# Kernel tuning notes

Hardware: AMD Instinct MI355X
Metric: run time of the kernel (lower is better)

## Reference

```python
import jax, jax.numpy as jnp
import numpy as np

IMG = 800.0
STRIDES = (4, 8, 16, 32)
SIZES = (32.0, 64.0, 128.0, 256.0)
RATIOS = (0.5, 1.0, 2.0)
A = 3
PRE_NMS_K = 1000
POST_NMS = 512
NMS_TH = 0.7
POOL = 7
_MEAN = np.array([0.485, 0.456, 0.406], np.float32).reshape(3, 1, 1)
_STD = np.array([0.229, 0.224, 0.225], np.float32).reshape(3, 1, 1)


def _conv(x, w, stride=1):
    # x: [C,H,W], w: [O,I,kh,kw]
    return jax.lax.conv_general_dilated(x[None], w, (stride, stride), 'SAME',
                                        dimension_numbers=('NCHW', 'OIHW', 'NCHW'))[0]


def _make_anchors(fh, fw, stride, size):
    cy = (np.arange(fh, dtype=np.float32) + 0.5) * stride
    cx = (np.arange(fw, dtype=np.float32) + 0.5) * stride
    ws = np.array([size / np.sqrt(r) for r in RATIOS], np.float32)
    hs = np.array([size * np.sqrt(r) for r in RATIOS], np.float32)
    gy, gx = np.meshgrid(cy, cx, indexing='ij')
    x1 = gx[..., None] - ws / 2; y1 = gy[..., None] - hs / 2
    x2 = gx[..., None] + ws / 2; y2 = gy[..., None] + hs / 2
    return jnp.asarray(np.stack([x1, y1, x2, y2], -1).reshape(-1, 4))  # [fh*fw*A,4]


def _decode(anchors, deltas):
    aw = anchors[:, 2] - anchors[:, 0]; ah = anchors[:, 3] - anchors[:, 1]
    acx = anchors[:, 0] + aw * 0.5; acy = anchors[:, 1] + ah * 0.5
    dw = jnp.clip(deltas[:, 2], -4.0, 4.0); dh = jnp.clip(deltas[:, 3], -4.0, 4.0)
    cx = acx + deltas[:, 0] * aw; cy = acy + deltas[:, 1] * ah
    w = aw * jnp.exp(dw); h = ah * jnp.exp(dh)
    boxes = jnp.stack([cx - w * 0.5, cy - h * 0.5, cx + w * 0.5, cy + h * 0.5], -1)
    return jnp.clip(boxes, 0.0, IMG)


def _nms(boxes, scores, iou_th, max_out):
    # Greedy NMS with fixed output size (jit-compatible).
    x1, y1, x2, y2 = boxes[:, 0], boxes[:, 1], boxes[:, 2], boxes[:, 3]
    areas = (x2 - x1) * (y2 - y1)

    def body(i, state):
        s, keep = state
        idx = jnp.argmax(s)
        keep = keep.at[i].set(idx)
        ix1 = jnp.maximum(x1, x1[idx]); iy1 = jnp.maximum(y1, y1[idx])
        ix2 = jnp.minimum(x2, x2[idx]); iy2 = jnp.minimum(y2, y2[idx])
        inter = jnp.maximum(ix2 - ix1, 0.0) * jnp.maximum(iy2 - iy1, 0.0)
        iou = inter / (areas + areas[idx] - inter + 1e-6)
        return jnp.where(iou > iou_th, -jnp.inf, s), keep

    _, keep = jax.lax.fori_loop(0, max_out, body, (scores, jnp.zeros(max_out, jnp.int32)))
    return keep


def _roi_align(feat, rois, scale):
    # feat: [C,H,W]; rois: [N,4] in image coords; bilinear, 1 sample per bin.
    C, H, W = feat.shape
    n = rois.shape[0]
    x1 = rois[:, 0] * scale; y1 = rois[:, 1] * scale
    bw = (rois[:, 2] - rois[:, 0]) * scale / POOL
    bh = (rois[:, 3] - rois[:, 1]) * scale / POOL
    j = jnp.arange(POOL, dtype=feat.dtype) + 0.5
    gx = jnp.broadcast_to((x1[:, None] + j * bw[:, None] - 0.5)[:, None, :], (n, POOL, POOL))
    gy = jnp.broadcast_to((y1[:, None] + j * bh[:, None] - 0.5)[:, :, None], (n, POOL, POOL))
    fx = jnp.clip(jnp.floor(gx), 0.0, W - 1); fy = jnp.clip(jnp.floor(gy), 0.0, H - 1)
    x0 = fx.astype(jnp.int32); y0 = fy.astype(jnp.int32)
    x1i = jnp.minimum(x0 + 1, W - 1); y1i = jnp.minimum(y0 + 1, H - 1)
    wx = jnp.clip(gx - fx, 0.0, 1.0); wy = jnp.clip(gy - fy, 0.0, 1.0)
    v = (feat[:, y0, x0] * (1 - wy) * (1 - wx) + feat[:, y0, x1i] * (1 - wy) * wx
         + feat[:, y1i, x0] * wy * (1 - wx) + feat[:, y1i, x1i] * wy * wx)  # [C,N,P,P]
    return jnp.transpose(v, (1, 0, 2, 3))  # [N,C,P,P]


def _forward(x, stem_w, c2_w, c3_w, c4_w, c5_w, fpn2_w, fpn3_w, fpn4_w, fpn5_w,
             rpn_w, rpn_cls_w, rpn_box_w, fc1_w, fc1_b, fc2_w, fc2_b,
             cls_w, cls_b, breg_w, breg_b):
    x = (x - _MEAN) / _STD  # ImageNet normalize
    h = jax.nn.relu(_conv(x, stem_w, 2))      # [64,400,400]
    c2 = jax.nn.relu(_conv(h, c2_w, 2))       # [256,200,200] stride 4
    c3 = jax.nn.relu(_conv(c2, c3_w, 2))      # stride 8
    c4 = jax.nn.relu(_conv(c3, c4_w, 2))      # stride 16
    c5 = jax.nn.relu(_conv(c4, c5_w, 2))      # stride 32
    feats = [_conv(c2, fpn2_w), _conv(c3, fpn3_w), _conv(c4, fpn4_w), _conv(c5, fpn5_w)]

    boxes_l, scores_l = [], []
    for lvl, f in enumerate(feats):
        t = jax.nn.relu(_conv(f, rpn_w))
        fh, fw = f.shape[1], f.shape[2]
        logits = jnp.transpose(_conv(t, rpn_cls_w), (1, 2, 0)).reshape(-1)  # [fh*fw*A]
        deltas = jnp.transpose(_conv(t, rpn_box_w).reshape(A, 4, fh, fw), (2, 3, 0, 1)).reshape(-1, 4)
        anchors = _make_anchors(fh, fw, STRIDES[lvl], SIZES[lvl])
        dec = _decode(anchors, deltas)
        k = min(PRE_NMS_K, logits.shape[0])
        sc, idx = jax.lax.top_k(logits, k)
        boxes_l.append(dec[idx]); scores_l.append(sc)

    boxes = jnp.concatenate(boxes_l, 0)
    scores = jnp.concatenate(scores_l, 0)
    keep = _nms(boxes, scores, NMS_TH, POST_NMS)
    props = boxes[keep]  # [POST_NMS,4]

    pooled = _roi_align(feats[0], props, 1.0 / STRIDES[0])  # [N,256,7,7]
    v = pooled.reshape(POST_NMS, -1)
    v = jax.nn.relu(v @ fc1_w + fc1_b)
    v = jax.nn.relu(v @ fc2_w + fc2_b)
    return v @ cls_w + cls_b, v @ breg_w + breg_b, props, scores[keep]


def setup_inputs() -> dict:
    key = jax.random.key(0)
    ks = jax.random.split(key, 18)

    def he(k, shape):
        fan_in = int(np.prod(shape[1:])) if len(shape) == 4 else shape[0]
        return jax.random.normal(k, shape, jnp.float32) * float(np.sqrt(2.0 / fan_in))

    inp = {'x': jax.random.uniform(ks[0], (3, 800, 800), jnp.float32)}
    inp['stem_w'] = he(ks[1], (64, 3, 7, 7))
    inp['c2_w'] = he(ks[2], (256, 64, 3, 3))
    for i, name in enumerate(['c3_w', 'c4_w', 'c5_w', 'fpn2_w', 'fpn3_w', 'fpn4_w', 'fpn5_w', 'rpn_w']):
        inp[name] = he(ks[3 + i], (256, 256, 3, 3))
    inp['rpn_cls_w'] = he(ks[11], (3, 256, 1, 1))
    inp['rpn_box_w'] = he(ks[12], (12, 256, 1, 1))
    inp['fc1_w'] = he(ks[13], (12544, 1024)); inp['fc1_b'] = jnp.zeros((1024,), jnp.float32)
    inp['fc2_w'] = he(ks[14], (1024, 1024)); inp['fc2_b'] = jnp.zeros((1024,), jnp.float32)
    inp['cls_w'] = he(ks[15], (1024, 2)); inp['cls_b'] = jnp.zeros((2,), jnp.float32)
    inp['breg_w'] = he(ks[16], (1024, 8)); inp['breg_b'] = jnp.zeros((8,), jnp.float32)
    return inp


def reference(x, stem_w, c2_w, c3_w, c4_w, c5_w, fpn2_w, fpn3_w, fpn4_w, fpn5_w,
              rpn_w, rpn_cls_w, rpn_box_w, fc1_w, fc1_b, fc2_w, fc2_b,
              cls_w, cls_b, breg_w, breg_b):
    return _forward(x, stem_w, c2_w, c3_w, c4_w, c5_w, fpn2_w, fpn3_w, fpn4_w, fpn5_w,
                    rpn_w, rpn_cls_w, rpn_box_w, fc1_w, fc1_b, fc2_w, fc2_b,
                    cls_w, cls_b, breg_w, breg_b)
```

## Files before the change

kernel.cpp:

```cpp
#include <hip/hip_runtime.h>
#include <math.h>


#define DI __device__ __forceinline__

typedef short short8 __attribute__((ext_vector_type(8)));
typedef float float16v __attribute__((ext_vector_type(16)));

DI unsigned fkey(float f) {
  unsigned u = __float_as_uint(f);
  return (u & 0x80000000u) ? ~u : (u | 0x80000000u);
}

DI unsigned short f2bf(float f) {
  unsigned u = __float_as_uint(f);
  unsigned r = (u + 0x7FFFu + ((u >> 16) & 1u)) >> 16;
  return (unsigned short)r;
}

__global__ __launch_bounds__(256) void stem_conv(const float* __restrict__ x,
                                                 const float* __restrict__ w,
                                                 float* __restrict__ out) {
  __shared__ float tin[3 * 37 * 37];
  __shared__ float tw[4 * 147];
  const int x0 = blockIdx.x * 16, y0 = blockIdx.y * 16, co0 = blockIdx.z * 4;
  const int tid = threadIdx.x;
  for (int i = tid; i < 4 * 147; i += 256) tw[i] = w[co0 * 147 + i];
  const int ix0 = x0 * 2 - 2, iy0 = y0 * 2 - 2;
  const float mean[3] = {0.485f, 0.456f, 0.406f};
  const float stdv[3] = {0.229f, 0.224f, 0.225f};
  for (int i = tid; i < 3 * 37 * 37; i += 256) {
    int c = i / 1369, r = i % 1369, yy = r / 37, xx = r % 37;
    int gy = iy0 + yy, gx = ix0 + xx;
    float v = 0.f;
    if ((unsigned)gy < 800u && (unsigned)gx < 800u)
      v = __fdiv_rn(__fsub_rn(x[c * 640000 + gy * 800 + gx], mean[c]), stdv[c]);
    tin[i] = v;
  }
  __syncthreads();
  const int tx = tid & 15, ty = tid >> 4;
  float acc[4] = {0.f, 0.f, 0.f, 0.f};
  for (int c = 0; c < 3; ++c)
    for (int ky = 0; ky < 7; ++ky)
#pragma unroll
      for (int kx = 0; kx < 7; ++kx) {
        float v = tin[c * 1369 + (ty * 2 + ky) * 37 + (tx * 2 + kx)];
#pragma unroll
        for (int co = 0; co < 4; ++co)
          acc[co] = fmaf(v, tw[co * 147 + c * 49 + ky * 7 + kx], acc[co]);
      }
  int ox = x0 + tx, oy = y0 + ty;
#pragma unroll
  for (int co = 0; co < 4; ++co)
    out[(size_t)(co0 + co) * 160000 + oy * 400 + ox] = fmaxf(acc[co], 0.f);
}

__global__ void repack_w32(const float* __restrict__ w,
                           float* __restrict__ wpk, int Cin) {
  int i = blockIdx.x * 256 + threadIdx.x;
  int total = 16 * Cin * 9 * 16;
  if (i >= total) return;
  int co = i & 15;
  int r = i >> 4;
  int kk = r % 9;
  int r2 = r / 9;
  int ci = r2 % Cin;
  int z = r2 / Cin;
  wpk[i] = w[((size_t)(z * 16 + co) * Cin + ci) * 9 + kk];
}

template <bool RELU>
__global__ __launch_bounds__(256) void conv32_db(
    const float* __restrict__ in, const float* __restrict__ wpk,
    float* __restrict__ out, int Cin, int Hin, int Win, int Hout, int Wout) {
  __shared__ __align__(16) float tin2[2][5120];
  const int tid = threadIdx.x;
  const int tx = tid & 15, ty = tid >> 4;
  const int x0 = blockIdx.x * 32, y0 = blockIdx.y * 16;
  const int ix0 = x0 - 1, iy0 = y0 - 1;
  const size_t HWin = (size_t)Hin * Win;

  int goff[20];
#pragma unroll
  for (int j = 0; j < 20; ++j) {
    int e = j * 256 + tid;
    int c = e / 612, r = e % 612;
    int yy = r / 34, xx = r % 34;
    int gy = iy0 + yy, gx = ix0 + xx;
    bool ok = (e < 4896) && ((unsigned)gy < (unsigned)Hin) &&
              ((unsigned)gx < (unsigned)Win);
    goff[j] = ok ? (int)((size_t)c * HWin + (size_t)gy * Win + gx) : -1;
  }

  float acc0[16], acc1[16];
#pragma unroll
  for (int co = 0; co < 16; ++co) { acc0[co] = 0.f; acc1[co] = 0.f; }

  float stg[20];
#pragma unroll
  for (int j = 0; j < 20; ++j)
    stg[j] = (goff[j] >= 0) ? in[goff[j]] : 0.f;
#pragma unroll
  for (int j = 0; j < 20; ++j) tin2[0][j * 256 + tid] = stg[j];
  __syncthreads();

  int buf = 0;
  for (int cb = 0; cb < Cin; cb += 8) {
    const bool more = (cb + 8) < Cin;
    if (more) {
      const float* gsrc = in + (size_t)(cb + 8) * HWin;
#pragma unroll
      for (int j = 0; j < 20; ++j)
        stg[j] = (goff[j] >= 0) ? gsrc[goff[j]] : 0.f;
    }
    for (int ci = 0; ci < 8; ++ci) {
      const float4* wq = (const float4*)(wpk +
          ((size_t)blockIdx.z * Cin + (size_t)(cb + ci)) * 144);
#pragma unroll
      for (int ky = 0; ky < 3; ++ky) {
        const float* tb = &tin2[buf][ci * 612 + (ty + ky) * 34 + 2 * tx];
        float2 d0 = *(const float2*)tb;
        float2 d1 = *(const float2*)(tb + 2);
#pragma unroll
        for (int kx = 0; kx < 3; ++kx) {
          float v0 = (kx == 0) ? d0.x : (kx == 1) ? d0.y : d1.x;
          float v1 = (kx == 0) ? d0.y : (kx == 1) ? d1.x : d1.y;
          const int kk = ky * 3 + kx;
          float4 w0 = wq[kk * 4 + 0];
          float4 w1 = wq[kk * 4 + 1];
          float4 w2 = wq[kk * 4 + 2];
          float4 w3 = wq[kk * 4 + 3];
          acc0[0]  = fmaf(v0, w0.x, acc0[0]);
          acc0[1]  = fmaf(v0, w0.y, acc0[1]);
          acc0[2]  = fmaf(v0, w0.z, acc0[2]);
          acc0[3]  = fmaf(v0, w0.w, acc0[3]);
          acc1[0]  = fmaf(v1, w0.x, acc1[0]);
          acc1[1]  = fmaf(v1, w0.y, acc1[1]);
          acc1[2]  = fmaf(v1, w0.z, acc1[2]);
          acc1[3]  = fmaf(v1, w0.w, acc1[3]);
          acc0[4]  = fmaf(v0, w1.x, acc0[4]);
          acc0[5]  = fmaf(v0, w1.y, acc0[5]);
          acc0[6]  = fmaf(v0, w1.z, acc0[6]);
          acc0[7]  = fmaf(v0, w1.w, acc0[7]);
          acc1[4]  = fmaf(v1, w1.x, acc1[4]);
          acc1[5]  = fmaf(v1, w1.y, acc1[5]);
          acc1[6]  = fmaf(v1, w1.z, acc1[6]);
          acc1[7]  = fmaf(v1, w1.w, acc1[7]);
          acc0[8]  = fmaf(v0, w2.x, acc0[8]);
          acc0[9]  = fmaf(v0, w2.y, acc0[9]);
          acc0[10] = fmaf(v0, w2.z, acc0[10]);
          acc0[11] = fmaf(v0, w2.w, acc0[11]);
          acc1[8]  = fmaf(v1, w2.x, acc1[8]);
          acc1[9]  = fmaf(v1, w2.y, acc1[9]);
          acc1[10] = fmaf(v1, w2.z, acc1[10]);
          acc1[11] = fmaf(v1, w2.w, acc1[11]);
          acc0[12] = fmaf(v0, w3.x, acc0[12]);
          acc0[13] = fmaf(v0, w3.y, acc0[13]);
          acc0[14] = fmaf(v0, w3.z, acc0[14]);
          acc0[15] = fmaf(v0, w3.w, acc0[15]);
          acc1[12] = fmaf(v1, w3.x, acc1[12]);
          acc1[13] = fmaf(v1, w3.y, acc1[13]);
          acc1[14] = fmaf(v1, w3.z, acc1[14]);
          acc1[15] = fmaf(v1, w3.w, acc1[15]);
        }
      }
    }
    if (more) {
#pragma unroll
      for (int j = 0; j < 20; ++j) tin2[buf ^ 1][j * 256 + tid] = stg[j];
    }
    __syncthreads();
    buf ^= 1;
  }

  const int co0 = blockIdx.z * 16;
  int oy = y0 + ty;
  if (oy < Hout) {
    int ox = x0 + 2 * tx;
    if (ox + 1 < Wout) {
#pragma unroll
      for (int co = 0; co < 16; ++co) {
        float a = acc0[co], b = acc1[co];
        if (RELU) { a = fmaxf(a, 0.f); b = fmaxf(b, 0.f); }
        float2 st; st.x = a; st.y = b;
        *(float2*)&out[(size_t)(co0 + co) * Hout * Wout +
                       (size_t)oy * Wout + ox] = st;
      }
    } else if (ox < Wout) {
#pragma unroll
      for (int co = 0; co < 16; ++co) {
        float a = acc0[co];
        if (RELU) a = fmaxf(a, 0.f);
        out[(size_t)(co0 + co) * Hout * Wout + (size_t)oy * Wout + ox] = a;
      }
    }
  }
}

template <int CHUNK, bool RELU>
__global__ __launch_bounds__(256) void conv16_s1(const float* __restrict__ in,
                                                 const float* __restrict__ wpk,
                                                 float* __restrict__ out,
                                                 int Cin, int Hin, int Win,
                                                 int Hout, int Wout) {
  constexpr int P = 24;
  constexpr int TOT = CHUNK * 18 * 18;
  constexpr int NS = (TOT + 255) / 256;
  __shared__ __align__(16) float tin[CHUNK * 18 * P];
  const int tid = threadIdx.x;
  const int tx = tid & 15, ty = tid >> 4;
  const int x0 = blockIdx.x * 16, y0 = blockIdx.y * 16;
  const int ix0 = x0 - 1, iy0 = y0 - 1;
  const size_t HWin = (size_t)Hin * Win;

  int goff[NS], loff[NS];
#pragma unroll
  for (int j = 0; j < NS; ++j) {
    int i = tid + j * 256;
    int c = i / 324, r = i % 324;
    int yy = r / 18, xx = r % 18;
    int gy = iy0 + yy, gx = ix0 + xx;
    bool ok = (i < TOT) && ((unsigned)gy < (unsigned)Hin) &&
              ((unsigned)gx < (unsigned)Win);
    goff[j] = ok ? (int)(c * HWin + (size_t)gy * Win + gx) : -1;
    loff[j] = c * 18 * P + yy * P + xx;
  }

  float acc[16];
#pragma unroll
  for (int co = 0; co < 16; ++co) acc[co] = 0.f;

  for (int cb = 0; cb < Cin; cb += CHUNK) {
    const size_t gbase = (size_t)cb * HWin;
#pragma unroll
    for (int j = 0; j < NS; ++j) {
      int i = tid + j * 256;
      if (i < TOT) {
        float v = 0.f;
        if (goff[j] >= 0) v = in[gbase + goff[j]];
        tin[loff[j]] = v;
      }
    }
    __syncthreads();
    for (int ci = 0; ci < CHUNK; ++ci) {
      const float4* wq = (const float4*)(wpk +
          ((size_t)blockIdx.z * Cin + (size_t)(cb + ci)) * 144);
#pragma unroll
      for (int ky = 0; ky < 3; ++ky) {
#pragma unroll
        for (int kx = 0; kx < 3; ++kx) {
          const int kk = ky * 3 + kx;
          float v = tin[ci * 18 * P + (ty + ky) * P + tx + kx];
          float4 w0 = wq[kk * 4 + 0];
          float4 w1 = wq[kk * 4 + 1];
          float4 w2 = wq[kk * 4 + 2];
          float4 w3 = wq[kk * 4 + 3];
          acc[0]  = fmaf(v, w0.x, acc[0]);
          acc[1]  = fmaf(v, w0.y, acc[1]);
          acc[2]  = fmaf(v, w0.z, acc[2]);
          acc[3]  = fmaf(v, w0.w, acc[3]);
          acc[4]  = fmaf(v, w1.x, acc[4]);
          acc[5]  = fmaf(v, w1.y, acc[5]);
          acc[6]  = fmaf(v, w1.z, acc[6]);
          acc[7]  = fmaf(v, w1.w, acc[7]);
          acc[8]  = fmaf(v, w2.x, acc[8]);
          acc[9]  = fmaf(v, w2.y, acc[9]);
          acc[10] = fmaf(v, w2.z, acc[10]);
          acc[11] = fmaf(v, w2.w, acc[11]);
          acc[12] = fmaf(v, w3.x, acc[12]);
          acc[13] = fmaf(v, w3.y, acc[13]);
          acc[14] = fmaf(v, w3.z, acc[14]);
          acc[15] = fmaf(v, w3.w, acc[15]);
        }
      }
    }
    __syncthreads();
  }
  const int co0 = blockIdx.z * 16;
  int oy = y0 + ty, ox = x0 + tx;
  if (oy < Hout && ox < Wout) {
#pragma unroll
    for (int co = 0; co < 16; ++co) {
      float v = acc[co];
      if (RELU) v = fmaxf(v, 0.f);
      out[(size_t)(co0 + co) * Hout * Wout + (size_t)oy * Wout + ox] = v;
    }
  }
}

template <int CHUNK, bool RELU>
__global__ __launch_bounds__(256) void conv16_s2(const float* __restrict__ in,
                                                 const float* __restrict__ wpk,
                                                 float* __restrict__ out,
                                                 int Cin, int Hin, int Win,
                                                 int Hout, int Wout) {
  constexpr int P = 20;
  constexpr int HALF = CHUNK * 33 * P;
  constexpr int TOT = CHUNK * 33 * 33;
  constexpr int NS = (TOT + 255) / 256;
  __shared__ __align__(16) float tin2[2 * HALF];
  const int tid = threadIdx.x;
  const int tx = tid & 15, ty = tid >> 4;
  const int x0 = blockIdx.x * 16, y0 = blockIdx.y * 16;
  const int ix0 = x0 * 2, iy0 = y0 * 2;
  const size_t HWin = (size_t)Hin * Win;

  int goff[NS], loff[NS];
#pragma unroll
  for (int j = 0; j < NS; ++j) {
    int i = tid + j * 256;
    int c = i / 1089, r = i % 1089;
    int yy = r / 33, xx = r % 33;
    int gy = iy0 + yy, gx = ix0 + xx;
    bool ok = (i < TOT) && ((unsigned)gy < (unsigned)Hin) &&
              ((unsigned)gx < (unsigned)Win);
    goff[j] = ok ? (int)(c * HWin + (size_t)gy * Win + gx) : -1;
    loff[j] = c * 33 * P + yy * P + (xx >> 1) + ((xx & 1) ? HALF : 0);
  }

  float acc[16];
#pragma unroll
  for (int co = 0; co < 16; ++co) acc[co] = 0.f;

  for (int cb = 0; cb < Cin; cb += CHUNK) {
    const size_t gbase = (size_t)cb * HWin;
#pragma unroll
    for (int j = 0; j < NS; ++j) {
      int i = tid + j * 256;
      if (i < TOT) {
        float v = 0.f;
        if (goff[j] >= 0) v = in[gbase + goff[j]];
        tin2[loff[j]] = v;
      }
    }
    __syncthreads();
    for (int ci = 0; ci < CHUNK; ++ci) {
      const float4* wq = (const float4*)(wpk +
          ((size_t)blockIdx.z * Cin + (size_t)(cb + ci)) * 144);
#pragma unroll
      for (int ky = 0; ky < 3; ++ky) {
#pragma unroll
        for (int kx = 0; kx < 3; ++kx) {
          const int kk = ky * 3 + kx;
          const float* base = (kx == 1) ? (tin2 + HALF) : tin2;
          const int cadd = (kx == 2) ? 1 : 0;
          float v = base[ci * 33 * P + (2 * ty + ky) * P + tx + cadd];
          float4 w0 = wq[kk * 4 + 0];
          float4 w1 = wq[kk * 4 + 1];
          float4 w2 = wq[kk * 4 + 2];
          float4 w3 = wq[kk * 4 + 3];
          acc[0]  = fmaf(v, w0.x, acc[0]);
          acc[1]  = fmaf(v, w0.y, acc[1]);
          acc[2]  = fmaf(v, w0.z, acc[2]);
          acc[3]  = fmaf(v, w0.w, acc[3]);
          acc[4]  = fmaf(v, w1.x, acc[4]);
          acc[5]  = fmaf(v, w1.y, acc[5]);
          acc[6]  = fmaf(v, w1.z, acc[6]);
          acc[7]  = fmaf(v, w1.w, acc[7]);
          acc[8]  = fmaf(v, w2.x, acc[8]);
          acc[9]  = fmaf(v, w2.y, acc[9]);
          acc[10] = fmaf(v, w2.z, acc[10]);
          acc[11] = fmaf(v, w2.w, acc[11]);
          acc[12] = fmaf(v, w3.x, acc[12]);
          acc[13] = fmaf(v, w3.y, acc[13]);
          acc[14] = fmaf(v, w3.z, acc[14]);
          acc[15] = fmaf(v, w3.w, acc[15]);
        }
      }
    }
    __syncthreads();
  }
  const int co0 = blockIdx.z * 16;
  int oy = y0 + ty, ox = x0 + tx;
  if (oy < Hout && ox < Wout) {
#pragma unroll
    for (int co = 0; co < 16; ++co) {
      float v = acc[co];
      if (RELU) v = fmaxf(v, 0.f);
      out[(size_t)(co0 + co) * Hout * Wout + (size_t)oy * Wout + ox] = v;
    }
  }
}

__global__ __launch_bounds__(256) void transpose_t(const float* __restrict__ in,
                                                   float* __restrict__ out,
                                                   int npix) {
  __shared__ float tile[32][33];
  const int p0 = blockIdx.x * 32, c0 = blockIdx.y * 32;
  const int tx = threadIdx.x & 31, ty = threadIdx.x >> 5;
  for (int r = ty; r < 32; r += 8) {
    int p = p0 + tx;
    tile[r][tx] = (p < npix) ? in[(size_t)(c0 + r) * npix + p] : 0.f;
  }
  __syncthreads();
  for (int r = ty; r < 32; r += 8) {
    int p = p0 + r;
    if (p < npix) out[(size_t)p * 256 + c0 + tx] = tile[tx][r];
  }
}

__global__ __launch_bounds__(256) void rpn_head_decode(
    const float* __restrict__ tt, const float* __restrict__ wcls,
    const float* __restrict__ wbox, float* __restrict__ boxes,
    float* __restrict__ scores, int fh, int fw, float stride, float ws0,
    float ws1, float ws2, float hs0, float hs1, float hs2) {
  __shared__ __align__(16) float wcs[256][16];
  for (int i = threadIdx.x; i < 256 * 16; i += 256) {
    int c = i & 255, o = i >> 8;
    float v = 0.f;
    if (o < 3) v = wcls[o * 256 + c];
    else if (o < 15) v = wbox[(o - 3) * 256 + c];
    wcs[c][o] = v;
  }
  __syncthreads();
  const int npix = fh * fw;
  int p = blockIdx.x * 256 + threadIdx.x;
  if (p >= npix) return;
  float a[15];
#pragma unroll
  for (int o = 0; o < 15; ++o) a[o] = 0.f;
  const float4* tp = (const float4*)(tt + (size_t)p * 256);
#pragma unroll 4
  for (int c4 = 0; c4 < 64; ++c4) {
    float4 tv = tp[c4];
#pragma unroll
    for (int j = 0; j < 4; ++j) {
      float v = (j == 0) ? tv.x : (j == 1) ? tv.y : (j == 2) ? tv.z : tv.w;
      int c = c4 * 4 + j;
      const float4* wr = (const float4*)&wcs[c][0];
      float4 w0 = wr[0], w1 = wr[1], w2 = wr[2], w3 = wr[3];
      a[0] = fmaf(v, w0.x, a[0]);   a[1] = fmaf(v, w0.y, a[1]);
      a[2] = fmaf(v, w0.z, a[2]);   a[3] = fmaf(v, w0.w, a[3]);
      a[4] = fmaf(v, w1.x, a[4]);   a[5] = fmaf(v, w1.y, a[5]);
      a[6] = fmaf(v, w1.z, a[6]);   a[7] = fmaf(v, w1.w, a[7]);
      a[8] = fmaf(v, w2.x, a[8]);   a[9] = fmaf(v, w2.y, a[9]);
      a[10] = fmaf(v, w2.z, a[10]); a[11] = fmaf(v, w2.w, a[11]);
      a[12] = fmaf(v, w3.x, a[12]); a[13] = fmaf(v, w3.y, a[13]);
      a[14] = fmaf(v, w3.z, a[14]);
    }
  }
  const int i = p / fw, j = p % fw;
  const float acy0 = __fmul_rn((float)i + 0.5f, stride);
  const float acx0 = __fmul_rn((float)j + 0.5f, stride);
  const float WS[3] = {ws0, ws1, ws2}, HS[3] = {hs0, hs1, hs2};
#pragma unroll
  for (int an = 0; an < 3; ++an) {
    float hw = __fmul_rn(WS[an], 0.5f), hh = __fmul_rn(HS[an], 0.5f);
    float x1a = __fsub_rn(acx0, hw), x2a = __fadd_rn(acx0, hw);
    float y1a = __fsub_rn(acy0, hh), y2a = __fadd_rn(acy0, hh);
    float aw = __fsub_rn(x2a, x1a), ah = __fsub_rn(y2a, y1a);
    float acx = __fadd_rn(x1a, __fmul_rn(aw, 0.5f));
    float acy = __fadd_rn(y1a, __fmul_rn(ah, 0.5f));
    float dx = a[3 + an * 4 + 0], dy = a[3 + an * 4 + 1];
    float dw = fminf(fmaxf(a[3 + an * 4 + 2], -4.f), 4.f);
    float dh = fminf(fmaxf(a[3 + an * 4 + 3], -4.f), 4.f);
    float cx = __fadd_rn(acx, __fmul_rn(dx, aw));
    float cy = __fadd_rn(acy, __fmul_rn(dy, ah));
    float w_ = __fmul_rn(aw, expf(dw));
    float h_ = __fmul_rn(ah, expf(dh));
    int idx = p * 3 + an;
    boxes[idx * 4 + 0] =
        fminf(fmaxf(__fsub_rn(cx, __fmul_rn(w_, 0.5f)), 0.f), 800.f);
    boxes[idx * 4 + 1] =
        fminf(fmaxf(__fsub_rn(cy, __fmul_rn(h_, 0.5f)), 0.f), 800.f);
    boxes[idx * 4 + 2] =
        fminf(fmaxf(__fadd_rn(cx, __fmul_rn(w_, 0.5f)), 0.f), 800.f);
    boxes[idx * 4 + 3] =
        fminf(fmaxf(__fadd_rn(cy, __fmul_rn(h_, 0.5f)), 0.f), 800.f);
    scores[idx] = a[an];
  }
}

__global__ void hist_hi_kernel(const float* __restrict__ s, int n,
                               int* __restrict__ hist) {
  int i = blockIdx.x * blockDim.x + threadIdx.x;
  if (i < n) atomicAdd(&hist[fkey(s[i]) >> 16], 1);
}

__global__ void hist_lo_kernel(const float* __restrict__ s, int n,
                               const int* __restrict__ sel,
                               int* __restrict__ hist) {
  unsigned b = (unsigned)sel[0];
  int i = blockIdx.x * blockDim.x + threadIdx.x;
  if (i < n) {
    unsigned key = fkey(s[i]);
    if ((key >> 16) == b) atomicAdd(&hist[key & 0xffffu], 1);
  }
}

__global__ __launch_bounds__(256) void scan_hi_kernel(
    const int* __restrict__ hist, int k, int* __restrict__ sel) {
  __shared__ int csum[256];
  int t = threadIdx.x;
  int s = 0;
  for (int i = 0; i < 256; ++i) s += hist[t * 256 + i];
  csum[t] = s;
  __syncthreads();
  if (t == 0) {
    int cum = 0;
    for (int c = 255; c >= 0; --c) {
      if (cum + csum[c] >= k) {
        int cc = cum;
        for (int b = c * 256 + 255;; --b) {
          int h = hist[b];
          if (cc + h >= k) {
            sel[0] = b; sel[1] = k - cc; sel[2] = cc;
            return;
          }
          cc += h;
        }
      }
      cum += csum[c];
    }
    sel[0] = 0; sel[1] = k - cum; sel[2] = cum;
  }
}

__global__ __launch_bounds__(256) void scan_lo_kernel(
    const int* __restrict__ hist, int* __restrict__ sel) {
  __shared__ int csum[256];
  int t = threadIdx.x;
  int s = 0;
  for (int i = 0; i < 256; ++i) s += hist[t * 256 + i];
  csum[t] = s;
  __syncthreads();
  if (t == 0) {
    int r = sel[1], b = sel[0], cc_hi = sel[2];
    int cum = 0;
    for (int c = 255; c >= 0; --c) {
      if (cum + csum[c] >= r) {
        int cc = cum;
        for (int l = c * 256 + 255;; --l) {
          int h = hist[l];
          if (cc + h >= r) {
            sel[3] = (int)(((unsigned)b << 16) | (unsigned)l);
            sel[4] = cc_hi + cc;
            sel[5] = r - cc;
            sel[6] = 0;
            sel[7] = 0;
            return;
          }
          cc += h;
        }
      }
      cum += csum[c];
    }
    sel[3] = (int)((unsigned)b << 16);
    sel[4] = cc_hi; sel[5] = r; sel[6] = 0; sel[7] = 0;
  }
}

__global__ void compact_kernel(const float* __restrict__ s,
                               const float* __restrict__ boxes, int n,
                               int* __restrict__ sel, float* __restrict__ out_s,
                               float* __restrict__ out_b, int obase) {
  int i = blockIdx.x * blockDim.x + threadIdx.x;
  if (i >= n) return;
  unsigned key = fkey(s[i]);
  unsigned kth = (unsigned)sel[3];
  int pos = -1;
  if (key > kth) {
    pos = atomicAdd(&sel[6], 1);
  } else if (key == kth) {
    int e = atomicAdd(&sel[7], 1);
    if (e < sel[5]) pos = sel[4] + e;
  }
  if (pos >= 0) {
    int o = obase + pos;
    out_s[o] = s[i];
    out_b[o * 4 + 0] = boxes[i * 4 + 0];
    out_b[o * 4 + 1] = boxes[i * 4 + 1];
    out_b[o * 4 + 2] = boxes[i * 4 + 2];
    out_b[o * 4 + 3] = boxes[i * 4 + 3];
  }
}

#define NMS_N 4000
#define NMS_W 63

__global__ __launch_bounds__(256) void rank_kernel(const float* __restrict__ s,
                                                   int* __restrict__ order) {
  __shared__ float ls[NMS_N];
  for (int i = threadIdx.x; i < NMS_N; i += 256) ls[i] = s[i];
  __syncthreads();
  int i = blockIdx.x * 256 + threadIdx.x;
  if (i >= NMS_N) return;
  float si = ls[i];
  int cnt = 0;
  for (int j = 0; j < NMS_N; ++j) {
    float sj = ls[j];
    cnt += (sj > si) || (sj == si && j < i);
  }
  order[cnt] = i;
}

__global__ __launch_bounds__(256) void supp_kernel(
    const float* __restrict__ boxes, unsigned long long* __restrict__ supp) {
  __shared__ float sx1[NMS_W * 64], sy1[NMS_W * 64];
  __shared__ float sx2[NMS_W * 64], sy2[NMS_W * 64];
  for (int i = threadIdx.x; i < NMS_W * 64; i += 256) {
    float x1 = 0.f, y1 = 0.f, x2 = 0.f, y2 = 0.f;
    if (i < NMS_N) {
      x1 = boxes[i * 4 + 0]; y1 = boxes[i * 4 + 1];
      x2 = boxes[i * 4 + 2]; y2 = boxes[i * 4 + 3];
    }
    sx1[i] = x1; sy1[i] = y1; sx2[i] = x2; sy2[i] = y2;
  }
  __syncthreads();
  const int wave = threadIdx.x >> 6, lane = threadIdx.x & 63;
  for (int rr = 0; rr < 16; ++rr) {
    int i = blockIdx.x * 16 + rr;
    if (i >= NMS_N) return;
    float ix1 = sx1[i], iy1 = sy1[i], ix2 = sx2[i], iy2 = sy2[i];
    float ia = __fmul_rn(__fsub_rn(ix2, ix1), __fsub_rn(iy2, iy1));
    for (int w = wave; w < NMS_W; w += 4) {
      int j = w * 64 + lane;
      float jx1 = sx1[j], jy1 = sy1[j], jx2 = sx2[j], jy2 = sy2[j];
      float ja = __fmul_rn(__fsub_rn(jx2, jx1), __fsub_rn(jy2, jy1));
      float cx1 = fmaxf(jx1, ix1), cy1 = fmaxf(jy1, iy1);
      float cx2 = fminf(jx2, ix2), cy2 = fminf(jy2, iy2);
      float iw = fmaxf(__fsub_rn(cx2, cx1), 0.f);
      float ih = fmaxf(__fsub_rn(cy2, cy1), 0.f);
      float inter = __fmul_rn(iw, ih);
      float denom = __fadd_rn(__fsub_rn(__fadd_rn(ja, ia), inter), 1e-6f);
      bool pred = __fdiv_rn(inter, denom) > 0.7f;
      unsigned long long bits = __ballot(pred);
      if (lane == 0) supp[(size_t)i * NMS_W + w] = bits;
    }
  }
}

__global__ __launch_bounds__(64) void nms_scan(
    const unsigned long long* __restrict__ supp, const int* __restrict__ order,
    const float* __restrict__ boxes, const float* __restrict__ scores,
    float* __restrict__ props, float* __restrict__ out_props,
    float* __restrict__ out_scores) {
  __shared__ unsigned long long removed[NMS_W];
  __shared__ int keepL[512];
  const int tid = threadIdx.x;
  if (tid < NMS_W) removed[tid] = 0ull;
  __syncthreads();
  int kept = 0, sticky = -1;
  for (int g = 0; g < NMS_W && sticky < 0 && kept < 512; ++g) {
    int pos = g * 64 + tid;
    int c = (pos < NMS_N) ? order[pos] : -1;
    while (kept < 512) {
      bool avail = (c >= 0) && !((removed[c >> 6] >> (c & 63)) & 1ull);
      unsigned long long bal = __ballot(avail);
      if (bal == 0ull) break;
      int fl = __ffsll((unsigned long long)bal) - 1;
      int ck = __shfl(c, fl);
      if (tid == 0) keepL[kept] = ck;
      kept++;
      unsigned long long w =
          (tid < NMS_W) ? supp[(size_t)ck * NMS_W + tid] : 0ull;
      unsigned long long selfw = __shfl(w, ck >> 6);
      if (tid < NMS_W) removed[tid] |= w;
      __syncthreads();
      if (!((selfw >> (ck & 63)) & 1ull)) { sticky = ck; break; }
    }
  }
  __syncthreads();
  const int fill = (sticky >= 0) ? sticky : 0;
  for (int k = tid; k < 512; k += 64) {
    int idx = (k < kept) ? keepL[k] : fill;
    float x1 = boxes[idx * 4 + 0], y1 = boxes[idx * 4 + 1];
    float x2 = boxes[idx * 4 + 2], y2 = boxes[idx * 4 + 3];
    props[k * 4 + 0] = x1; props[k * 4 + 1] = y1;
    props[k * 4 + 2] = x2; props[k * 4 + 3] = y2;
    out_props[k * 4 + 0] = x1; out_props[k * 4 + 1] = y1;
    out_props[k * 4 + 2] = x2; out_props[k * 4 + 3] = y2;
    out_scores[k] = scores[idx];
  }
}

__global__ __launch_bounds__(256) void roi_align_kernel(
    const float* __restrict__ feat, const float* __restrict__ rois,
    float* __restrict__ out) {
  __shared__ int sx0[7], sx1i[7], sy0[7], sy1i[7];
  __shared__ float swx[7], swy[7];
  const int n = blockIdx.x;
  if (threadIdx.x < 14) {
    int i = threadIdx.x % 7;
    bool isY = threadIdx.x >= 7;
    float r0 = rois[n * 4 + (isY ? 1 : 0)];
    float r1 = rois[n * 4 + (isY ? 3 : 2)];
    float a = __fmul_rn(r0, 0.25f);
    float b = __fdiv_rn(__fmul_rn(__fsub_rn(r1, r0), 0.25f), 7.0f);
    float g = __fsub_rn(__fadd_rn(a, __fmul_rn((float)i + 0.5f, b)), 0.5f);
    float fl = fminf(fmaxf(floorf(g), 0.f), 199.f);
    int i0 = (int)fl;
    int i1 = min(i0 + 1, 199);
    float wf = fminf(fmaxf(__fsub_rn(g, fl), 0.f), 1.f);
    if (isY) { sy0[i] = i0; sy1i[i] = i1; swy[i] = wf; }
    else     { sx0[i] = i0; sx1i[i] = i1; swx[i] = wf; }
  }
  __syncthreads();
  const int c = threadIdx.x;
  const float* fc_ = feat + (size_t)c * 40000;
  float* o = out + (size_t)n * 12544 + c * 49;
  for (int s = 0; s < 49; ++s) {
    int py = s / 7, px = s % 7;
    int y0 = sy0[py], y1 = sy1i[py], x0 = sx0[px], x1 = sx1i[px];
    float wy = swy[py], wx = swx[px];
    float v00 = fc_[y0 * 200 + x0], v01 = fc_[y0 * 200 + x1];
    float v10 = fc_[y1 * 200 + x0], v11 = fc_[y1 * 200 + x1];
    float v = ((v00 * (1.f - wy)) * (1.f - wx)) + ((v01 * (1.f - wy)) * wx) +
              ((v10 * wy) * (1.f - wx)) + ((v11 * wy) * wx);
    o[s] = v;
  }
}

__global__ void cast_a(const float* __restrict__ in,
                       unsigned short* __restrict__ out, int n) {
  int i = blockIdx.x * 256 + threadIdx.x;
  if (i < n) out[i] = f2bf(in[i]);
}

__global__ __launch_bounds__(256) void cast_bt(const float* __restrict__ B,
                                               unsigned short* __restrict__ Bt,
                                               int K, int N) {
  __shared__ float tile[32][33];
  const int k0 = blockIdx.y * 32, n0 = blockIdx.x * 32;
  const int tx = threadIdx.x & 31, ty = threadIdx.x >> 5;
  for (int r = ty; r < 32; r += 8)
    tile[r][tx] = B[(size_t)(k0 + r) * N + n0 + tx];
  __syncthreads();
  for (int r = ty; r < 32; r += 8)
    Bt[(size_t)(n0 + r) * K + k0 + tx] = f2bf(tile[tx][r]);
}

__global__ __launch_bounds__(256) void fc_mfma(
    const unsigned short* __restrict__ A,
    const unsigned short* __restrict__ Bt,
    float* __restrict__ Cp, int M, int N, int K, int kLen) {
  const int tid = threadIdx.x;
  const int lane = tid & 63, wave = tid >> 6;
  const int n = lane & 31, half = lane >> 5;
  const int bm = blockIdx.y * 128 + wave * 32;
  const int bn = blockIdx.x * 64;
  const int k0s = blockIdx.z * kLen;
  const unsigned short* arow = A + (size_t)(bm + n) * K + half * 8;
  const unsigned short* b0row = Bt + (size_t)(bn + n) * K + half * 8;
  const unsigned short* b1row = Bt + (size_t)(bn + 32 + n) * K + half * 8;
  float16v acc0, acc1;
#pragma unroll
  for (int r = 0; r < 16; ++r) { acc0[r] = 0.f; acc1[r] = 0.f; }
  for (int k0 = k0s; k0 < k0s + kLen; k0 += 16) {
    short8 a = *(const short8*)(arow + k0);
    short8 b0 = *(const short8*)(b0row + k0);
    short8 b1 = *(const short8*)(b1row + k0);
    acc0 = __builtin_amdgcn_mfma_f32_32x32x16_bf16(a, b0, acc0, 0, 0, 0);
    acc1 = __builtin_amdgcn_mfma_f32_32x32x16_bf16(a, b1, acc1, 0, 0, 0);
  }
  float* Cz = Cp + (size_t)blockIdx.z * M * N;
#pragma unroll
  for (int r = 0; r < 16; ++r) {
    int row = bm + (r & 3) + 8 * (r >> 2) + 4 * half;
    Cz[(size_t)row * N + bn + n] = acc0[r];
    Cz[(size_t)row * N + bn + 32 + n] = acc1[r];
  }
}

__global__ void fc_combine(const float* __restrict__ p,
                           const float* __restrict__ bias,
                           float* __restrict__ out, int MN, int N, int S) {
  int i = blockIdx.x * 256 + threadIdx.x;
  if (i >= MN) return;
  float v = 0.f;
  for (int s = 0; s < S; ++s) v += p[(size_t)s * MN + i];
  out[i] = fmaxf(v + bias[i % N], 0.f);
}

__global__ __launch_bounds__(64) void heads_kernel(
    const float* __restrict__ v, const float* __restrict__ wc,
    const float* __restrict__ bc, const float* __restrict__ wb,
    const float* __restrict__ bbias, float* __restrict__ out) {
  const int m = blockIdx.x;
  const int lane = threadIdx.x;
  float acc[10];
#pragma unroll
  for (int o = 0; o < 10; ++o) acc[o] = 0.f;
  for (int k = lane; k < 1024; k += 64) {
    float x = v[(size_t)m * 1024 + k];
    acc[0] = fmaf(x, wc[k * 2 + 0], acc[0]);
    acc[1] = fmaf(x, wc[k * 2 + 1], acc[1]);
#pragma unroll
    for (int o = 0; o < 8; ++o) acc[2 + o] = fmaf(x, wb[k * 8 + o], acc[2 + o]);
  }
#pragma unroll
  for (int off = 32; off > 0; off >>= 1)
#pragma unroll
    for (int o = 0; o < 10; ++o) acc[o] += __shfl_down(acc[o], off);
  if (lane == 0) {
    out[m * 2 + 0] = acc[0] + bc[0];
    out[m * 2 + 1] = acc[1] + bc[1];
#pragma unroll
    for (int o = 0; o < 8; ++o) out[1024 + m * 8 + o] = acc[2 + o] + bbias[o];
  }
}

extern "C" void kernel_launch(void* const* d_in, const int* in_sizes, int n_in,
                              void* d_out, int out_size, void* d_ws,
                              size_t ws_size, hipStream_t stream) {
  const float* x      = (const float*)d_in[0];
  const float* w_stem = (const float*)d_in[1];
  const float* w_c2   = (const float*)d_in[2];
  const float* w_c3   = (const float*)d_in[3];
  const float* w_c4   = (const float*)d_in[4];
  const float* w_c5   = (const float*)d_in[5];
  const float* w_f2   = (const float*)d_in[6];
  const float* w_f3   = (const float*)d_in[7];
  const float* w_f4   = (const float*)d_in[8];
  const float* w_f5   = (const float*)d_in[9];
  const float* w_rpn  = (const float*)d_in[10];
  const float* w_cls  = (const float*)d_in[11];
  const float* w_box  = (const float*)d_in[12];
  const float* w_fc1  = (const float*)d_in[13];
  const float* b_fc1  = (const float*)d_in[14];
  const float* w_fc2  = (const float*)d_in[15];
  const float* b_fc2  = (const float*)d_in[16];
  const float* w_clsh = (const float*)d_in[17];
  const float* b_clsh = (const float*)d_in[18];
  const float* w_breg = (const float*)d_in[19];
  const float* b_breg = (const float*)d_in[20];
  float* dout = (float*)d_out;

  float* ws = (float*)d_ws;
  float* stem = ws;
  float* c2   = stem + 10240000;
  float* c3   = c2 + 10240000;
  float* c4   = c3 + 2560000;
  float* c5   = c4 + 640000;
  float* f2   = c5 + 160000;
  float* f3   = f2 + 10240000;
  float* f4   = f3 + 2560000;
  float* f5   = f4 + 640000;
  float* boxes_all  = f5 + 160000;
  float* scores_all = boxes_all + 16000;
  float* props      = scores_all + 4000;
  int*   hist = (int*)(props + 2048);
  int*   sel  = hist + 65536;
  float* wpkA = (float*)(sel + 16);
  float* wpkB = wpkA + 589824;
  float* wpkC = wpkB + 589824;
  float* wpkD = wpkC + 589824;
  float* wpkE = wpkD + 147456;
  float* wpkF = wpkE + 589824;
  float* wpkG = wpkF + 589824;
  float* wpkH = wpkG + 589824;
  float* wpkI = wpkH + 589824;
  float* t      = c2;
  float* tt     = stem;
  float* dec    = c3;
  float* slvl   = c4;
  int*   order  = (int*)c3;
  unsigned long long* supp =
      (unsigned long long*)(c3 + 8192);
  float* pooled = stem;
  float* fc1o   = stem + 6422528;
  float* fc2o   = fc1o + 524288;
  float* fcp    = fc2o + 524288;
  unsigned short* Abf1 = (unsigned short*)c2;
  unsigned short* Bt1  = (unsigned short*)(c2 + 3211264);
  unsigned short* Abf2 = (unsigned short*)c3;
  unsigned short* Bt2  = (unsigned short*)(c3 + 262144);

  repack_w32<<<2304, 256, 0, stream>>>(w_f2, wpkA, 256);
  repack_w32<<<2304, 256, 0, stream>>>(w_f3, wpkB, 256);
  repack_w32<<<2304, 256, 0, stream>>>(w_rpn, wpkC, 256);
  repack_w32<<<576, 256, 0, stream>>>(w_c2, wpkD, 64);
  repack_w32<<<2304, 256, 0, stream>>>(w_c3, wpkE, 256);
  repack_w32<<<2304, 256, 0, stream>>>(w_c4, wpkF, 256);
  repack_w32<<<2304, 256, 0, stream>>>(w_c5, wpkG, 256);
  repack_w32<<<2304, 256, 0, stream>>>(w_f4, wpkH, 256);
  repack_w32<<<2304, 256, 0, stream>>>(w_f5, wpkI, 256);

  stem_conv<<<dim3(25, 25, 16), 256, 0, stream>>>(x, w_stem, stem);
  conv16_s2<4, true><<<dim3(13, 13, 16), 256, 0, stream>>>(
      stem, wpkD, c2, 64, 400, 400, 200, 200);
  conv16_s2<4, true><<<dim3(7, 7, 16), 256, 0, stream>>>(
      c2, wpkE, c3, 256, 200, 200, 100, 100);
  conv16_s2<4, true><<<dim3(4, 4, 16), 256, 0, stream>>>(
      c3, wpkF, c4, 256, 100, 100, 50, 50);
  conv16_s2<4, true><<<dim3(2, 2, 16), 256, 0, stream>>>(
      c4, wpkG, c5, 256, 50, 50, 25, 25);
  conv32_db<false><<<dim3(7, 13, 16), 256, 0, stream>>>(
      c2, wpkA, f2, 256, 200, 200, 200, 200);
  conv32_db<false><<<dim3(4, 7, 16), 256, 0, stream>>>(
      c3, wpkB, f3, 256, 100, 100, 100, 100);
  conv16_s1<8, false><<<dim3(4, 4, 16), 256, 0, stream>>>(
      c4, wpkH, f4, 256, 50, 50, 50, 50);
  conv16_s1<8, false><<<dim3(2, 2, 16), 256, 0, stream>>>(
      c5, wpkI, f5, 256, 25, 25, 25, 25);

  const float* feats[4] = {f2, f3, f4, f5};
  const int dims[4] = {200, 100, 50, 25};
  const float strds[4] = {4.f, 8.f, 16.f, 32.f};
  const double szs[4] = {32.0, 64.0, 128.0, 256.0};
  for (int lvl = 0; lvl < 4; ++lvl) {
    const int d = dims[lvl];
    const int npix = d * d;
    const int N = npix * 3;
    if (lvl == 0)
      conv32_db<true><<<dim3(7, 13, 16), 256, 0, stream>>>(
          feats[lvl], wpkC, t, 256, d, d, d, d);
    else if (lvl == 1)
      conv32_db<true><<<dim3(4, 7, 16), 256, 0, stream>>>(
          feats[lvl], wpkC, t, 256, d, d, d, d);
    else if (lvl == 2)
      conv16_s1<8, true><<<dim3(4, 4, 16), 256, 0, stream>>>(
          feats[lvl], wpkC, t, 256, d, d, d, d);
    else
      conv16_s1<8, true><<<dim3(2, 2, 16), 256, 0, stream>>>(
          feats[lvl], wpkC, t, 256, d, d, d, d);
    transpose_t<<<dim3((npix + 31) / 32, 8), 256, 0, stream>>>(t, tt, npix);
    double sz = szs[lvl];
    float ws0 = (float)(sz / sqrt(0.5)), ws1 = (float)sz,
          ws2 = (float)(sz / sqrt(2.0));
    float hs0 = (float)(sz * sqrt(0.5)), hs1 = (float)sz,
          hs2 = (float)(sz * sqrt(2.0));
    rpn_head_decode<<<(npix + 255) / 256, 256, 0, stream>>>(
        tt, w_cls, w_box, dec, slvl, d, d, strds[lvl], ws0, ws1, ws2, hs0, hs1,
        hs2);
    hipMemsetAsync(hist, 0, 65536 * sizeof(int), stream);
    hist_hi_kernel<<<(N + 255) / 256, 256, 0, stream>>>(slvl, N, hist);
    scan_hi_kernel<<<1, 256, 0, stream>>>(hist, 1000, sel);
    hipMemsetAsync(hist, 0, 65536 * sizeof(int), stream);
    hist_lo_kernel<<<(N + 255) / 256, 256, 0, stream>>>(slvl, N, sel, hist);
    scan_lo_kernel<<<1, 256, 0, stream>>>(hist, sel);
    compact_kernel<<<(N + 255) / 256, 256, 0, stream>>>(
        slvl, dec, N, sel, scores_all, boxes_all, lvl * 1000);
  }

  rank_kernel<<<16, 256, 0, stream>>>(scores_all, order);
  supp_kernel<<<250, 256, 0, stream>>>(boxes_all, supp);
  nms_scan<<<1, 64, 0, stream>>>(supp, order, boxes_all, scores_all, props,
                                 dout + 5120, dout + 7168);

  roi_align_kernel<<<512, 256, 0, stream>>>(f2, props, pooled);
  cast_a<<<(6422528 + 255) / 256, 256, 0, stream>>>(pooled, Abf1, 6422528);
  cast_bt<<<dim3(32, 392), 256, 0, stream>>>(w_fc1, Bt1, 12544, 1024);
  fc_mfma<<<dim3(16, 4, 4), 256, 0, stream>>>(Abf1, Bt1, fcp, 512, 1024, 12544,
                                              3136);
  fc_combine<<<2048, 256, 0, stream>>>(fcp, b_fc1, fc1o, 524288, 1024, 4);
  cast_a<<<(524288 + 255) / 256, 256, 0, stream>>>(fc1o, Abf2, 524288);
  cast_bt<<<dim3(32, 32), 256, 0, stream>>>(w_fc2, Bt2, 1024, 1024);
  fc_mfma<<<dim3(16, 4, 4), 256, 0, stream>>>(Abf2, Bt2, fcp, 512, 1024, 1024,
                                              256);
  fc_combine<<<2048, 256, 0, stream>>>(fcp, b_fc2, fc2o, 524288, 1024, 4);
  heads_kernel<<<512, 64, 0, stream>>>(fc2o, w_clsh, b_clsh, w_breg, b_breg,
                                       dout);
}
```

Before: 5.374 ms.

## Compute 32 output channels per conv block and fuse histogram into RPN decode

The double-buffered 3x3 conv kernel now computes two 16-channel groups per block, halving the z grid so each staged input tile is reused for twice as many output channels. This doubles the accumulator registers to 64 per thread, which may lower occupancy. Separately, the high-bits histogram is built inside rpn_head_decode, replacing a separate kernel launch and a second pass over the scores. The scan kernels now zero the histogram themselves, so two memsets per level become one memset before the loop.

```diff
diff --git a/kernel.cpp b/kernel.cpp
--- a/kernel.cpp
+++ b/kernel.cpp
@@ -79,6 +79,7 @@
   const int x0 = blockIdx.x * 32, y0 = blockIdx.y * 16;
   const int ix0 = x0 - 1, iy0 = y0 - 1;
   const size_t HWin = (size_t)Hin * Win;
+  const int zA = blockIdx.z * 2, zB = zA + 1;
 
   int goff[20];
 #pragma unroll
@@ -92,9 +93,11 @@
     goff[j] = ok ? (int)((size_t)c * HWin + (size_t)gy * Win + gx) : -1;
   }
 
-  float acc0[16], acc1[16];
-#pragma unroll
-  for (int co = 0; co < 16; ++co) { acc0[co] = 0.f; acc1[co] = 0.f; }
+  float accA0[16], accA1[16], accB0[16], accB1[16];
+#pragma unroll
+  for (int co = 0; co < 16; ++co) {
+    accA0[co] = 0.f; accA1[co] = 0.f; accB0[co] = 0.f; accB1[co] = 0.f;
+  }
 
   float stg[20];
 #pragma unroll
@@ -114,8 +117,10 @@
         stg[j] = (goff[j] >= 0) ? gsrc[goff[j]] : 0.f;
     }
     for (int ci = 0; ci < 8; ++ci) {
-      const float4* wq = (const float4*)(wpk +
-          ((size_t)blockIdx.z * Cin + (size_t)(cb + ci)) * 144);
+      const float4* wqA = (const float4*)(wpk +
+          ((size_t)zA * Cin + (size_t)(cb + ci)) * 144);
+      const float4* wqB = (const float4*)(wpk +
+          ((size_t)zB * Cin + (size_t)(cb + ci)) * 144);
 #pragma unroll
       for (int ky = 0; ky < 3; ++ky) {
         const float* tb = &tin2[buf][ci * 612 + (ty + ky) * 34 + 2 * tx];
@@ -126,42 +131,30 @@
           float v0 = (kx == 0) ? d0.x : (kx == 1) ? d0.y : d1.x;
           float v1 = (kx == 0) ? d0.y : (kx == 1) ? d1.x : d1.y;
           const int kk = ky * 3 + kx;
-          float4 w0 = wq[kk * 4 + 0];
-          float4 w1 = wq[kk * 4 + 1];
-          float4 w2 = wq[kk * 4 + 2];
-          float4 w3 = wq[kk * 4 + 3];
-          acc0[0]  = fmaf(v0, w0.x, acc0[0]);
-          acc0[1]  = fmaf(v0, w0.y, acc0[1]);
-          acc0[2]  = fmaf(v0, w0.z, acc0[2]);
-          acc0[3]  = fmaf(v0, w0.w, acc0[3]);
-          acc1[0]  = fmaf(v1, w0.x, acc1[0]);
-          acc1[1]  = fmaf(v1, w0.y, acc1[1]);
-          acc1[2]  = fmaf(v1, w0.z, acc1[2]);
-          acc1[3]  = fmaf(v1, w0.w, acc1[3]);
-          acc0[4]  = fmaf(v0, w1.x, acc0[4]);
-          acc0[5]  = fmaf(v0, w1.y, acc0[5]);
-          acc0[6]  = fmaf(v0, w1.z, acc0[6]);
-          acc0[7]  = fmaf(v0, w1.w, acc0[7]);
-          acc1[4]  = fmaf(v1, w1.x, acc1[4]);
-          acc1[5]  = fmaf(v1, w1.y, acc1[5]);
-          acc1[6]  = fmaf(v1, w1.z, acc1[6]);
-          acc1[7]  = fmaf(v1, w1.w, acc1[7]);
-          acc0[8]  = fmaf(v0, w2.x, acc0[8]);
-          acc0[9]  = fmaf(v0, w2.y, acc0[9]);
-          acc0[10] = fmaf(v0, w2.z, acc0[10]);
-          acc0[11] = fmaf(v0, w2.w, acc0[11]);
-          acc1[8]  = fmaf(v1, w2.x, acc1[8]);
-          acc1[9]  = fmaf(v1, w2.y, acc1[9]);
-          acc1[10] = fmaf(v1, w2.z, acc1[10]);
-          acc1[11] = fmaf(v1, w2.w, acc1[11]);
-          acc0[12] = fmaf(v0, w3.x, acc0[12]);
-          acc0[13] = fmaf(v0, w3.y, acc0[13]);
-          acc0[14] = fmaf(v0, w3.z, acc0[14]);
-          acc0[15] = fmaf(v0, w3.w, acc0[15]);
-          acc1[12] = fmaf(v1, w3.x, acc1[12]);
-          acc1[13] = fmaf(v1, w3.y, acc1[13]);
-          acc1[14] = fmaf(v1, w3.z, acc1[14]);
-          acc1[15] = fmaf(v1, w3.w, acc1[15]);
+#pragma unroll
+          for (int g = 0; g < 4; ++g) {
+            float4 w = wqA[kk * 4 + g];
+            accA0[g * 4 + 0] = fmaf(v0, w.x, accA0[g * 4 + 0]);
+            accA0[g * 4 + 1] = fmaf(v0, w.y, accA0[g * 4 + 1]);
+            accA0[g * 4 + 2] = fmaf(v0, w.z, accA0[g * 4 + 2]);
+            accA0[g * 4 + 3] = fmaf(v0, w.w, accA0[g * 4 + 3]);
+            accA1[g * 4 + 0] = fmaf(v1, w.x, accA1[g * 4 + 0]);
+            accA1[g * 4 + 1] = fmaf(v1, w.y, accA1[g * 4 + 1]);
+            accA1[g * 4 + 2] = fmaf(v1, w.z, accA1[g * 4 + 2]);
+            accA1[g * 4 + 3] = fmaf(v1, w.w, accA1[g * 4 + 3]);
+          }
+#pragma unroll
+          for (int g = 0; g < 4; ++g) {
+            float4 w = wqB[kk * 4 + g];
+            accB0[g * 4 + 0] = fmaf(v0, w.x, accB0[g * 4 + 0]);
+            accB0[g * 4 + 1] = fmaf(v0, w.y, accB0[g * 4 + 1]);
+            accB0[g * 4 + 2] = fmaf(v0, w.z, accB0[g * 4 + 2]);
+            accB0[g * 4 + 3] = fmaf(v0, w.w, accB0[g * 4 + 3]);
+            accB1[g * 4 + 0] = fmaf(v1, w.x, accB1[g * 4 + 0]);
+            accB1[g * 4 + 1] = fmaf(v1, w.y, accB1[g * 4 + 1]);
+            accB1[g * 4 + 2] = fmaf(v1, w.z, accB1[g * 4 + 2]);
+            accB1[g * 4 + 3] = fmaf(v1, w.w, accB1[g * 4 + 3]);
+          }
         }
       }
     }
@@ -173,25 +166,39 @@
     buf ^= 1;
   }
 
-  const int co0 = blockIdx.z * 16;
+  const int co0 = blockIdx.z * 32;
   int oy = y0 + ty;
   if (oy < Hout) {
     int ox = x0 + 2 * tx;
     if (ox + 1 < Wout) {
 #pragma unroll
       for (int co = 0; co < 16; ++co) {
-        float a = acc0[co], b = acc1[co];
+        float a = accA0[co], b = accA1[co];
         if (RELU) { a = fmaxf(a, 0.f); b = fmaxf(b, 0.f); }
         float2 st; st.x = a; st.y = b;
         *(float2*)&out[(size_t)(co0 + co) * Hout * Wout +
                        (size_t)oy * Wout + ox] = st;
       }
+#pragma unroll
+      for (int co = 0; co < 16; ++co) {
+        float a = accB0[co], b = accB1[co];
+        if (RELU) { a = fmaxf(a, 0.f); b = fmaxf(b, 0.f); }
+        float2 st; st.x = a; st.y = b;
+        *(float2*)&out[(size_t)(co0 + 16 + co) * Hout * Wout +
+                       (size_t)oy * Wout + ox] = st;
+      }
     } else if (ox < Wout) {
 #pragma unroll
       for (int co = 0; co < 16; ++co) {
-        float a = acc0[co];
+        float a = accA0[co];
         if (RELU) a = fmaxf(a, 0.f);
         out[(size_t)(co0 + co) * Hout * Wout + (size_t)oy * Wout + ox] = a;
+      }
+#pragma unroll
+      for (int co = 0; co < 16; ++co) {
+        float a = accB0[co];
+        if (RELU) a = fmaxf(a, 0.f);
+        out[(size_t)(co0 + 16 + co) * Hout * Wout + (size_t)oy * Wout + ox] = a;
       }
     }
   }
@@ -402,8 +409,9 @@
 __global__ __launch_bounds__(256) void rpn_head_decode(
     const float* __restrict__ tt, const float* __restrict__ wcls,
     const float* __restrict__ wbox, float* __restrict__ boxes,
-    float* __restrict__ scores, int fh, int fw, float stride, float ws0,
-    float ws1, float ws2, float hs0, float hs1, float hs2) {
+    float* __restrict__ scores, int* __restrict__ hist, int fh, int fw,
+    float stride, float ws0, float ws1, float ws2, float hs0, float hs1,
+    float hs2) {
   __shared__ __align__(16) float wcs[256][16];
   for (int i = threadIdx.x; i < 256 * 16; i += 256) {
     int c = i & 255, o = i >> 8;
@@ -468,13 +476,8 @@
     boxes[idx * 4 + 3] =
         fminf(fmaxf(__fadd_rn(cy, __fmul_rn(h_, 0.5f)), 0.f), 800.f);
     scores[idx] = a[an];
-  }
-}
-
-__global__ void hist_hi_kernel(const float* __restrict__ s, int n,
-                               int* __restrict__ hist) {
-  int i = blockIdx.x * blockDim.x + threadIdx.x;
-  if (i < n) atomicAdd(&hist[fkey(s[i]) >> 16], 1);
+    atomicAdd(&hist[fkey(a[an]) >> 16], 1);
+  }
 }
 
 __global__ void hist_lo_kernel(const float* __restrict__ s, int n,
@@ -489,7 +492,7 @@
 }
 
 __global__ __launch_bounds__(256) void scan_hi_kernel(
-    const int* __restrict__ hist, int k, int* __restrict__ sel) {
+    int* __restrict__ hist, int k, int* __restrict__ sel) {
   __shared__ int csum[256];
   int t = threadIdx.x;
   int s = 0;
@@ -498,6 +501,7 @@
   __syncthreads();
   if (t == 0) {
     int cum = 0;
+    bool done = false;
     for (int c = 255; c >= 0; --c) {
       if (cum + csum[c] >= k) {
         int cc = cum;
@@ -505,19 +509,24 @@
           int h = hist[b];
           if (cc + h >= k) {
             sel[0] = b; sel[1] = k - cc; sel[2] = cc;
-            return;
+            done = true;
+            break;
           }
           cc += h;
         }
+        break;
       }
       cum += csum[c];
     }
-    sel[0] = 0; sel[1] = k - cum; sel[2] = cum;
-  }
+    if (!done) { sel[0] = 0; sel[1] = k - cum; sel[2] = cum; }
+  }
+  __syncthreads();
+  int4 z4; z4.x = 0; z4.y = 0; z4.z = 0; z4.w = 0;
+  for (int i = t; i < 16384; i += 256) ((int4*)hist)[i] = z4;
 }
 
 __global__ __launch_bounds__(256) void scan_lo_kernel(
-    const int* __restrict__ hist, int* __restrict__ sel) {
+    int* __restrict__ hist, int* __restrict__ sel) {
   __shared__ int csum[256];
   int t = threadIdx.x;
   int s = 0;
@@ -527,6 +536,7 @@
   if (t == 0) {
     int r = sel[1], b = sel[0], cc_hi = sel[2];
     int cum = 0;
+    bool done = false;
     for (int c = 255; c >= 0; --c) {
       if (cum + csum[c] >= r) {
         int cc = cum;
@@ -538,16 +548,23 @@
             sel[5] = r - cc;
             sel[6] = 0;
             sel[7] = 0;
-            return;
+            done = true;
+            break;
           }
           cc += h;
         }
+        break;
       }
       cum += csum[c];
     }
-    sel[3] = (int)((unsigned)b << 16);
-    sel[4] = cc_hi; sel[5] = r; sel[6] = 0; sel[7] = 0;
-  }
+    if (!done) {
+      sel[3] = (int)((unsigned)b << 16);
+      sel[4] = cc_hi; sel[5] = r; sel[6] = 0; sel[7] = 0;
+    }
+  }
+  __syncthreads();
+  int4 z4; z4.x = 0; z4.y = 0; z4.z = 0; z4.w = 0;
+  for (int i = t; i < 16384; i += 256) ((int4*)hist)[i] = z4;
 }
 
 __global__ void compact_kernel(const float* __restrict__ s,
@@ -885,15 +902,16 @@
       c3, wpkF, c4, 256, 100, 100, 50, 50);
   conv16_s2<4, true><<<dim3(2, 2, 16), 256, 0, stream>>>(
       c4, wpkG, c5, 256, 50, 50, 25, 25);
-  conv32_db<false><<<dim3(7, 13, 16), 256, 0, stream>>>(
+  conv32_db<false><<<dim3(7, 13, 8), 256, 0, stream>>>(
       c2, wpkA, f2, 256, 200, 200, 200, 200);
-  conv32_db<false><<<dim3(4, 7, 16), 256, 0, stream>>>(
+  conv32_db<false><<<dim3(4, 7, 8), 256, 0, stream>>>(
       c3, wpkB, f3, 256, 100, 100, 100, 100);
   conv16_s1<8, false><<<dim3(4, 4, 16), 256, 0, stream>>>(
       c4, wpkH, f4, 256, 50, 50, 50, 50);
   conv16_s1<8, false><<<dim3(2, 2, 16), 256, 0, stream>>>(
       c5, wpkI, f5, 256, 25, 25, 25, 25);
 
+  hipMemsetAsync(hist, 0, 65536 * sizeof(int), stream);
   const float* feats[4] = {f2, f3, f4, f5};
   const int dims[4] = {200, 100, 50, 25};
   const float strds[4] = {4.f, 8.f, 16.f, 32.f};
@@ -903,10 +921,10 @@
     const int npix = d * d;
     const int N = npix * 3;
     if (lvl == 0)
-      conv32_db<true><<<dim3(7, 13, 16), 256, 0, stream>>>(
+      conv32_db<true><<<dim3(7, 13, 8), 256, 0, stream>>>(
           feats[lvl], wpkC, t, 256, d, d, d, d);
     else if (lvl == 1)
-      conv32_db<true><<<dim3(4, 7, 16), 256, 0, stream>>>(
+      conv32_db<true><<<dim3(4, 7, 8), 256, 0, stream>>>(
           feats[lvl], wpkC, t, 256, d, d, d, d);
     else if (lvl == 2)
       conv16_s1<8, true><<<dim3(4, 4, 16), 256, 0, stream>>>(
@@ -921,12 +939,9 @@
     float hs0 = (float)(sz * sqrt(0.5)), hs1 = (float)sz,
           hs2 = (float)(sz * sqrt(2.0));
     rpn_head_decode<<<(npix + 255) / 256, 256, 0, stream>>>(
-        tt, w_cls, w_box, dec, slvl, d, d, strds[lvl], ws0, ws1, ws2, hs0, hs1,
-        hs2);
-    hipMemsetAsync(hist, 0, 65536 * sizeof(int), stream);
-    hist_hi_kernel<<<(N + 255) / 256, 256, 0, stream>>>(slvl, N, hist);
+        tt, w_cls, w_box, dec, slvl, hist, d, d, strds[lvl], ws0, ws1, ws2,
+        hs0, hs1, hs2);
     scan_hi_kernel<<<1, 256, 0, stream>>>(hist, 1000, sel);
-    hipMemsetAsync(hist, 0, 65536 * sizeof(int), stream);
     hist_lo_kernel<<<(N + 255) / 256, 256, 0, stream>>>(slvl, N, sel, hist);
     scan_lo_kernel<<<1, 256, 0, stream>>>(hist, sel);
     compact_kernel<<<(N + 255) / 256, 256, 0, stream>>>(
```

New measurement: 6.266 ms. +16.6%, slower.
